# Kernel tuning notes

Measured on AMD Instinct MI355X. Metric: run time of the kernel, lower is better.

## Reference

```python
import jax, jax.numpy as jnp
import numpy as np

SIZE = 161          # odd box size (init arg 160 -> 161)
INPUT_SIZE = 8
BATCH = 256
MARGIN = 3          # VOXEL_SPREAD_MARGIN


def _radial_expansion(grid):
    # verbatim numpy port of SparseVolumeReconstructionLinear.radial_expansion
    bz = grid.shape[0]
    bz2 = bz // 2
    mask1 = grid == -1
    ls = np.linspace(-bz2, bz2, bz)
    lsx = np.linspace(0, bz2, bz // 2 + 1)
    z, y, x = np.meshgrid(ls, ls, lsx)
    c = np.zeros((int(np.sum(mask1)), 3))
    c[:, 0] = x[mask1]
    c[:, 1] = y[mask1]
    c[:, 2] = z[mask1]
    norm = np.sqrt(np.sum(np.square(c), axis=1))
    c_ = np.round(c / norm[:, None]).astype(int)
    c = c.astype(int)
    c[:, 1:] += bz2
    c_ = c - c_
    g = grid[c_[:, 2], c_[:, 1], c_[:, 0]]
    mask2 = g >= 0
    grid[c[mask2, 2], c[mask2, 1], c[mask2, 0]] = g[mask2]


def _build_grid3d_index(size):
    bz = size
    bz_2 = bz // 2
    zz = (np.arange(bz) - bz_2) ** 2
    yy = (np.arange(bz) - bz_2) ** 2
    xx = np.arange(bz_2 + 1) ** 2
    mask = (zz[:, None, None] + yy[None, :, None] + xx[None, None, :]) <= bz_2 ** 2
    # C-order enumeration matches grid_iterator(z, y, x) ordering
    idx = np.cumsum(mask.ravel()).reshape(mask.shape) - 1
    grid = np.where(mask, idx, -1).astype(np.int64)
    m = MARGIN
    bzm = bz + 2 * m
    gm = np.full((bzm, bzm, bzm // 2 + 1), -1, dtype=np.int64)
    gm[m:-m, m:-m, :-m] = grid
    for _ in range(5):
        _radial_expansion(gm)
    return gm, int(mask.sum())


def _rand_rotations(key, n):
    q = jax.random.normal(key, (n, 4))
    q = q / jnp.linalg.norm(q, axis=1, keepdims=True)
    w, x, y, z = q[:, 0], q[:, 1], q[:, 2], q[:, 3]
    R = jnp.stack([
        1 - 2 * (y * y + z * z), 2 * (x * y - z * w), 2 * (x * z + y * w),
        2 * (x * y + z * w), 1 - 2 * (x * x + z * z), 2 * (y * z - x * w),
        2 * (x * z - y * w), 2 * (y * z + x * w), 1 - 2 * (x * x + y * y),
    ], axis=-1).reshape(n, 3, 3)
    return R.astype(jnp.float32)


def setup_inputs() -> dict:
    key = jax.random.key(0)
    k1, k2, k3, k4 = jax.random.split(key, 4)
    grid3d_index, weight_count = _build_grid3d_index(SIZE)
    weight = jax.random.normal(k1, (weight_count, INPUT_SIZE, 2), dtype=jnp.float32) * 1e-3
    bias = jax.random.normal(k2, (weight_count, 2), dtype=jnp.float32) * 1e-3
    inp = jax.random.normal(k3, (BATCH, INPUT_SIZE), dtype=jnp.float32)
    rot = _rand_rotations(k4, BATCH)
    # half-plane 2D Fourier coords (x >= 0), P = SIZE * (SIZE//2 + 1)
    ys, xs = np.meshgrid(np.arange(SIZE) - SIZE // 2, np.arange(SIZE // 2 + 1), indexing='ij')
    coord = np.stack([xs.ravel(), ys.ravel()], axis=-1).astype(np.float32)
    return {
        'input': inp,
        'weight': weight,
        'bias': bias,
        'grid3d_index': jnp.asarray(grid3d_index),
        'rot_matrices': rot,
        'grid2d_coord': jnp.asarray(coord),
        'max_r': SIZE // 2,
    }


def reference(input, weight, bias, grid3d_index, rot_matrices, grid2d_coord, max_r):
    # input: (B, D); weight: (W, D, 2); bias: (W, 2)
    # grid2d_coord: (P, 2) as (x, y); rot_matrices: (B, 3, 3)
    bz = grid3d_index.shape[0]
    bz2 = bz // 2
    mr = min(int(max_r), (bz - 2 * MARGIN) // 2)
    P = grid2d_coord.shape[0]
    # rotate the z=0 plane into 3D Fourier space: (B, P, 3) as (x, y, z)
    c2 = jnp.pad(grid2d_coord, ((0, 0), (0, 1)))
    c = jnp.einsum('bij,pj->bpi', rot_matrices, c2)
    # Hermitian symmetry: flip to x >= 0 half-grid, conjugate
    flip = c[..., 0] < 0
    c = jnp.where(flip[..., None], -c, c)
    valid = jnp.sum(grid2d_coord ** 2, axis=-1) <= float(mr * mr)  # (P,)
    c = jnp.where(valid[None, :, None], c, 0.0)
    f = jnp.floor(c)
    t = c - f                      # trilinear fractions (B, P, 3)
    fi = f.astype(jnp.int32)
    out = jnp.zeros((c.shape[0], P, 2), dtype=input.dtype)
    for dx in (0, 1):
        wx = t[..., 0] if dx else 1.0 - t[..., 0]
        for dy in (0, 1):
            wy = t[..., 1] if dy else 1.0 - t[..., 1]
            for dz in (0, 1):
                wz = t[..., 2] if dz else 1.0 - t[..., 2]
                xi = fi[..., 0] + dx
                yi = fi[..., 1] + dy + bz2
                zi = fi[..., 2] + dz + bz2
                j = grid3d_index[zi, yi, xi]        # (B, P) voxel ids, -1 = empty
                jm = jnp.maximum(j, 0)
                v = jnp.einsum('bd,bpdc->bpc', input, weight[jm]) + bias[jm]
                v = jnp.where((j >= 0)[..., None], v, 0.0)
                out = out + (wx * wy * wz)[..., None] * v
    imag_sign = jnp.where(flip, -1.0, 1.0)
    out = out * jnp.stack([jnp.ones_like(imag_sign), imag_sign], axis=-1)
    return jnp.where(valid[None, :, None], out, 0.0)
```

## Files before the change

kernel.cpp:

```cpp
#include <hip/hip_runtime.h>

#define BZ    167
#define BZ2   83
#define NX    84
#define NCELL (BZ * BZ * NX)
#define NBX   51
#define NBX2  102

static __device__ __forceinline__ unsigned f2bf(float f) {
    unsigned u = __float_as_uint(f);
    return (u + 0x7FFFu + ((u >> 16) & 1u)) >> 16;
}
static __device__ __forceinline__ float bf_lo(unsigned u) {
    return __uint_as_float(u << 16);
}
static __device__ __forceinline__ float bf_hi(unsigned u) {
    return __uint_as_float(u & 0xFFFF0000u);
}

__global__ __launch_bounds__(256) void pack_all(
    const float4* __restrict__ wsrc, uint2* __restrict__ wdst, int nw4, int nbw,
    const int* __restrict__ grid, const float* __restrict__ bias,
    int2* __restrict__ garr, int ncell)
{
    if ((int)blockIdx.x < nbw) {
        const int i = blockIdx.x * 256 + threadIdx.x;
        if (i >= nw4) return;
        const float4 v = wsrc[i];
        wdst[i] = make_uint2(f2bf(v.x) | (f2bf(v.y) << 16),
                             f2bf(v.z) | (f2bf(v.w) << 16));
    } else {
        const int i = ((int)blockIdx.x - nbw) * 256 + threadIdx.x;
        if (i >= ncell) return;
        const int j = grid[i];
        unsigned bb = 0u;
        if (j >= 0)
            bb = f2bf(bias[2 * j]) | (f2bf(bias[2 * j + 1]) << 16);
        garr[i] = make_int2(j, (int)bb);
    }
}

__global__ __launch_bounds__(256, 4) void svr_half(
    const float*    __restrict__ input,
    const unsigned* __restrict__ wpk,
    const int2*     __restrict__ garr,
    const float*    __restrict__ rot,
    const float*    __restrict__ coord,
    const int*      __restrict__ max_r,
    float*          __restrict__ out,
    int P)
{
    const int m    = blockIdx.x;
    const int xcd  = m & 7;
    const int slot = m >> 3;
    const int b    = (slot / NBX2) * 8 + xcd;
    const int lane = threadIdx.x;
    const int half = lane & 1;
    const int p    = (slot % NBX2) * 128 + (lane >> 1);
    if (p >= P) return;

    const float2 xy = *(const float2*)(coord + 2 * p);
    const float x = xy.x, y = xy.y;

    const int mr = min(max_r[0], (BZ - 6) / 2);
    const bool valid = (x * x + y * y) <= (float)(mr * mr);

    float* o = out + (((size_t)b * P + p) * 2 + half);
    if (!valid) {
        *o = 0.f;
        return;
    }

    const float* R = rot + b * 9;
    float cx = fmaf(R[1], y, R[0] * x);
    float cy = fmaf(R[4], y, R[3] * x);
    float cz = fmaf(R[7], y, R[6] * x);

    float sgn = 1.f;
    if (cx < 0.f) { cx = -cx; cy = -cy; cz = -cz; sgn = -1.f; }

    const float fx = floorf(cx), fy = floorf(cy), fz = floorf(cz);
    const float tx = cx - fx, ty = cy - fy, tz = cz - fz;
    const int ix = (int)fx;
    const int iy = (int)fy + BZ2;
    const int iz = (int)fz + BZ2;

    const float4 ih = *(const float4*)(input + b * 8 + half * 4);

    int2 G[8];
    #pragma unroll
    for (int dz = 0; dz < 2; ++dz) {
        #pragma unroll
        for (int dy = 0; dy < 2; ++dy) {
            const int base = ((iz + dz) * BZ + (iy + dy)) * NX + ix;
            const int c = dz * 4 + dy * 2;
            G[c + 0] = garr[base + 0];
            G[c + 1] = garr[base + 1];
        }
    }

    int   jj[8];
    float wc[8];
    {
        const float wx0 = 1.f - tx, wy0 = 1.f - ty, wz0 = 1.f - tz;
        #pragma unroll
        for (int c = 0; c < 8; ++c) {
            const int dx = c & 1, dy = (c >> 1) & 1, dz = c >> 2;
            const float w = (dx ? tx : wx0) * (dy ? ty : wy0) * (dz ? tz : wz0);
            const int j = G[c].x;
            wc[c] = (j >= 0) ? w : 0.f;
            jj[c] = max(j, 0);
        }
    }

    uint4 U[8];
    #pragma unroll
    for (int c = 0; c < 8; ++c)
        U[c] = *(const uint4*)(wpk + (size_t)jj[c] * 8 + half * 4);

    float acc0 = 0.f, acc1 = 0.f;
    #pragma unroll
    for (int c = 0; c < 8; ++c) {
        const float w = wc[c];
        const unsigned bb = (unsigned)G[c].y;
        float v0 = half ? 0.f : bf_lo(bb);
        float v1 = half ? 0.f : bf_hi(bb);
        v0 = fmaf(ih.x, bf_lo(U[c].x), v0); v1 = fmaf(ih.x, bf_hi(U[c].x), v1);
        v0 = fmaf(ih.y, bf_lo(U[c].y), v0); v1 = fmaf(ih.y, bf_hi(U[c].y), v1);
        v0 = fmaf(ih.z, bf_lo(U[c].z), v0); v1 = fmaf(ih.z, bf_hi(U[c].z), v1);
        v0 = fmaf(ih.w, bf_lo(U[c].w), v0); v1 = fmaf(ih.w, bf_hi(U[c].w), v1);
        acc0 = fmaf(w, v0, acc0);
        acc1 = fmaf(w, v1, acc1);
    }

    const float t0 = acc0 + __shfl_xor(acc0, 1);
    const float t1 = (acc1 + __shfl_xor(acc1, 1)) * sgn;
    *o = half ? t1 : t0;
}

__global__ __launch_bounds__(256) void pack_w(
    const float4* __restrict__ src, uint2* __restrict__ dst, int n)
{
    const int i = blockIdx.x * 256 + threadIdx.x;
    if (i >= n) return;
    const float4 v = src[i];
    dst[i] = make_uint2(f2bf(v.x) | (f2bf(v.y) << 16),
                        f2bf(v.z) | (f2bf(v.w) << 16));
}
__global__ __launch_bounds__(256) void pack_b(
    const float* __restrict__ bias, unsigned* __restrict__ bpk, int W)
{
    const int j = blockIdx.x * 256 + threadIdx.x;
    if (j >= W) return;
    bpk[j] = f2bf(bias[2 * j]) | (f2bf(bias[2 * j + 1]) << 16);
}

__global__ __launch_bounds__(256) void svr_bf16(
    const float* __restrict__ input, const unsigned* __restrict__ wpk,
    const unsigned* __restrict__ bpk, const int* __restrict__ grid3d,
    const float* __restrict__ rot, const float* __restrict__ coord,
    const int* __restrict__ max_r, float* __restrict__ out, int P)
{
    const int m    = blockIdx.x;
    const int xcd  = m & 7;
    const int slot = m >> 3;
    const int b    = (slot / NBX) * 8 + xcd;
    const int p    = (slot % NBX) * 256 + threadIdx.x;
    if (p >= P) return;

    const float x = coord[2 * p + 0];
    const float y = coord[2 * p + 1];
    const int mr = min(max_r[0], (BZ - 6) / 2);
    const bool valid = (x * x + y * y) <= (float)(mr * mr);
    float2* o = (float2*)(out + ((size_t)b * P + p) * 2);
    if (!valid) { *o = make_float2(0.f, 0.f); return; }

    const float* R = rot + b * 9;
    float cx = fmaf(R[1], y, R[0] * x);
    float cy = fmaf(R[4], y, R[3] * x);
    float cz = fmaf(R[7], y, R[6] * x);
    float sgn = 1.f;
    if (cx < 0.f) { cx = -cx; cy = -cy; cz = -cz; sgn = -1.f; }
    const float fx = floorf(cx), fy = floorf(cy), fz = floorf(cz);
    const float tx = cx - fx, ty = cy - fy, tz = cz - fz;
    const int ix = (int)fx, iy = (int)fy + BZ2, iz = (int)fz + BZ2;

    const float* ib = input + b * 8;
    const float in0 = ib[0], in1 = ib[1], in2 = ib[2], in3 = ib[3];
    const float in4 = ib[4], in5 = ib[5], in6 = ib[6], in7 = ib[7];

    int jj[8]; float wc[8];
    const float wx0 = 1.f - tx, wy0 = 1.f - ty, wz0 = 1.f - tz;
    #pragma unroll
    for (int dz = 0; dz < 2; ++dz)
        #pragma unroll
        for (int dy = 0; dy < 2; ++dy) {
            const int base = ((iz + dz) * BZ + (iy + dy)) * NX + ix;
            #pragma unroll
            for (int dx = 0; dx < 2; ++dx) {
                const int c = dz * 4 + dy * 2 + dx;
                const int j = grid3d[base + dx];
                const float w = (dx ? tx : wx0) * (dy ? ty : wy0) * (dz ? tz : wz0);
                wc[c] = (j >= 0) ? w : 0.f;
                jj[c] = max(j, 0);
            }
        }

    uint4 U0[8], U1[8]; unsigned BB[8];
    #pragma unroll
    for (int c = 0; c < 8; ++c) {
        const uint4* wp = (const uint4*)(wpk + (size_t)jj[c] * 8);
        U0[c] = wp[0]; U1[c] = wp[1]; BB[c] = bpk[jj[c]];
    }

    float acc0 = 0.f, acc1 = 0.f;
    #pragma unroll
    for (int c = 0; c < 8; ++c) {
        const float w = wc[c];
        float v0 = bf_lo(BB[c]), v1 = bf_hi(BB[c]);
        v0 = fmaf(in0, bf_lo(U0[c].x), v0); v1 = fmaf(in0, bf_hi(U0[c].x), v1);
        v0 = fmaf(in1, bf_lo(U0[c].y), v0); v1 = fmaf(in1, bf_hi(U0[c].y), v1);
        v0 = fmaf(in2, bf_lo(U0[c].z), v0); v1 = fmaf(in2, bf_hi(U0[c].z), v1);
        v0 = fmaf(in3, bf_lo(U0[c].w), v0); v1 = fmaf(in3, bf_hi(U0[c].w), v1);
        v0 = fmaf(in4, bf_lo(U1[c].x), v0); v1 = fmaf(in4, bf_hi(U1[c].x), v1);
        v0 = fmaf(in5, bf_lo(U1[c].y), v0); v1 = fmaf(in5, bf_hi(U1[c].y), v1);
        v0 = fmaf(in6, bf_lo(U1[c].z), v0); v1 = fmaf(in6, bf_hi(U1[c].z), v1);
        v0 = fmaf(in7, bf_lo(U1[c].w), v0); v1 = fmaf(in7, bf_hi(U1[c].w), v1);
        acc0 = fmaf(w, v0, acc0);
        acc1 = fmaf(w, v1, acc1);
    }
    *o = make_float2(acc0, acc1 * sgn);
}

__global__ __launch_bounds__(256) void svr_fp32(
    const float* __restrict__ input, const float* __restrict__ weight,
    const float* __restrict__ bias, const int* __restrict__ grid3d,
    const float* __restrict__ rot, const float* __restrict__ coord,
    const int* __restrict__ max_r, float* __restrict__ out, int P)
{
    const int m    = blockIdx.x;
    const int xcd  = m & 7;
    const int slot = m >> 3;
    const int b    = (slot / NBX) * 8 + xcd;
    const int p    = (slot % NBX) * 256 + threadIdx.x;
    if (p >= P) return;

    const float x = coord[2 * p + 0];
    const float y = coord[2 * p + 1];
    const int mr = min(max_r[0], (BZ - 6) / 2);
    const bool valid = (x * x + y * y) <= (float)(mr * mr);
    float2* o = (float2*)(out + ((size_t)b * P + p) * 2);
    if (!valid) { *o = make_float2(0.f, 0.f); return; }

    const float* R = rot + b * 9;
    float cx = fmaf(R[1], y, R[0] * x);
    float cy = fmaf(R[4], y, R[3] * x);
    float cz = fmaf(R[7], y, R[6] * x);
    float sgn = 1.f;
    if (cx < 0.f) { cx = -cx; cy = -cy; cz = -cz; sgn = -1.f; }
    const float fx = floorf(cx), fy = floorf(cy), fz = floorf(cz);
    const float tx = cx - fx, ty = cy - fy, tz = cz - fz;
    const int ix = (int)fx, iy = (int)fy + BZ2, iz = (int)fz + BZ2;

    const float* ib = input + b * 8;
    const float in0 = ib[0], in1 = ib[1], in2 = ib[2], in3 = ib[3];
    const float in4 = ib[4], in5 = ib[5], in6 = ib[6], in7 = ib[7];

    int jj[8]; float wc[8];
    const float wx0 = 1.f - tx, wy0 = 1.f - ty, wz0 = 1.f - tz;
    #pragma unroll
    for (int dz = 0; dz < 2; ++dz)
        #pragma unroll
        for (int dy = 0; dy < 2; ++dy) {
            const int base = ((iz + dz) * BZ + (iy + dy)) * NX + ix;
            #pragma unroll
            for (int dx = 0; dx < 2; ++dx) {
                const int c = dz * 4 + dy * 2 + dx;
                const int j = grid3d[base + dx];
                const float w = (dx ? tx : wx0) * (dy ? ty : wy0) * (dz ? tz : wz0);
                wc[c] = (j >= 0) ? w : 0.f;
                jj[c] = max(j, 0);
            }
        }

    float acc0 = 0.f, acc1 = 0.f;
    #pragma unroll
    for (int c = 0; c < 8; ++c) {
        const size_t j = (size_t)jj[c];
        const float4* wp = (const float4*)(weight + j * 16);
        const float4 W0 = wp[0], W1 = wp[1], W2 = wp[2], W3 = wp[3];
        const float2 bb = *(const float2*)(bias + j * 2);
        const float w = wc[c];
        float v0 = bb.x, v1 = bb.y;
        v0 = fmaf(in0, W0.x, v0); v1 = fmaf(in0, W0.y, v1);
        v0 = fmaf(in1, W0.z, v0); v1 = fmaf(in1, W0.w, v1);
        v0 = fmaf(in2, W1.x, v0); v1 = fmaf(in2, W1.y, v1);
        v0 = fmaf(in3, W1.z, v0); v1 = fmaf(in3, W1.w, v1);
        v0 = fmaf(in4, W2.x, v0); v1 = fmaf(in4, W2.y, v1);
        v0 = fmaf(in5, W2.z, v0); v1 = fmaf(in5, W2.w, v1);
        v0 = fmaf(in6, W3.x, v0); v1 = fmaf(in6, W3.y, v1);
        v0 = fmaf(in7, W3.z, v0); v1 = fmaf(in7, W3.w, v1);
        acc0 = fmaf(w, v0, acc0);
        acc1 = fmaf(w, v1, acc1);
    }
    *o = make_float2(acc0, acc1 * sgn);
}

extern "C" void kernel_launch(void* const* d_in, const int* in_sizes, int n_in,
                              void* d_out, int out_size, void* d_ws, size_t ws_size,
                              hipStream_t stream) {
    const float* input  = (const float*)d_in[0];
    const float* weight = (const float*)d_in[1];
    const float* bias   = (const float*)d_in[2];
    const int*   grid3d = (const int*)  d_in[3];
    const float* rot    = (const float*)d_in[4];
    const float* coord  = (const float*)d_in[5];
    const int*   max_r  = (const int*)  d_in[6];
    float* out = (float*)d_out;

    const int P = in_sizes[5] / 2;
    const int B = in_sizes[4] / 9;
    const int W = in_sizes[1] / 16;

    const size_t wpk_bytes  = (size_t)W * 32;
    const size_t garr_bytes = (size_t)NCELL * 8;
    const size_t need_full  = wpk_bytes + garr_bytes;
    const size_t need_bf    = (size_t)W * 36;

    dim3 block(256, 1, 1);

    if (ws_size >= need_full) {
        unsigned* wpk = (unsigned*)d_ws;
        int2* garr = (int2*)((char*)d_ws + wpk_bytes);
        const int nw4 = W * 4;
        const int nbw = (nw4 + 255) / 256;
        const int nbg = (NCELL + 255) / 256;
        pack_all<<<nbw + nbg, block, 0, stream>>>(
            (const float4*)weight, (uint2*)wpk, nw4, nbw,
            grid3d, bias, garr, NCELL);
        dim3 grid(NBX2 * B, 1, 1);
        svr_half<<<grid, block, 0, stream>>>(input, wpk, garr, rot, coord,
                                             max_r, out, P);
    } else if (ws_size >= need_bf) {
        unsigned* wpk = (unsigned*)d_ws;
        unsigned* bpk = wpk + (size_t)W * 8;
        const int nw = W * 4;
        pack_w<<<(nw + 255) / 256, block, 0, stream>>>(
            (const float4*)weight, (uint2*)wpk, nw);
        pack_b<<<(W + 255) / 256, block, 0, stream>>>(bias, bpk, W);
        dim3 grid(NBX * B, 1, 1);
        svr_bf16<<<grid, block, 0, stream>>>(input, wpk, bpk, grid3d, rot,
                                             coord, max_r, out, P);
    } else {
        dim3 grid(NBX * B, 1, 1);
        svr_fp32<<<grid, block, 0, stream>>>(input, weight, bias, grid3d, rot,
                                             coord, max_r, out, P);
    }
}
```

Baseline: 234.7 us.

## Split each output point across four lanes with paired x-neighbor grid table

Adds a new path in which each output point is handled by four lanes: two for the x-neighbor and two for each half of the input dimension. A shuffle reduction combines the partial sums. A new packing kernel builds a 16-byte table that stores the voxel id and packed bias for a cell and its +x neighbor, so the four y/z corners need only four gathers. This is meant to raise parallelism and cut serial gather latency per thread. In exchange the grid table doubles in size and the pack pass does more work.

```diff
diff --git a/kernel.cpp b/kernel.cpp
--- a/kernel.cpp
+++ b/kernel.cpp
@@ -6,6 +6,7 @@
 #define NCELL (BZ * BZ * NX)
 #define NBX   51
 #define NBX2  102
+#define NBQ   204
 
 static __device__ __forceinline__ unsigned f2bf(float f) {
     unsigned u = __float_as_uint(f);
@@ -16,6 +17,131 @@
 }
 static __device__ __forceinline__ float bf_hi(unsigned u) {
     return __uint_as_float(u & 0xFFFF0000u);
+}
+
+__global__ __launch_bounds__(256) void pack_all2(
+    const float4* __restrict__ wsrc, uint2* __restrict__ wdst, int nw4, int nbw,
+    const int* __restrict__ grid, const float* __restrict__ bias,
+    int4* __restrict__ gpair, int ncell)
+{
+    if ((int)blockIdx.x < nbw) {
+        const int i = blockIdx.x * 256 + threadIdx.x;
+        if (i >= nw4) return;
+        const float4 v = wsrc[i];
+        wdst[i] = make_uint2(f2bf(v.x) | (f2bf(v.y) << 16),
+                             f2bf(v.z) | (f2bf(v.w) << 16));
+    } else {
+        const int i = ((int)blockIdx.x - nbw) * 256 + threadIdx.x;
+        if (i >= ncell) return;
+        const int j0 = grid[i];
+        const int j1 = (i + 1 < ncell) ? grid[i + 1] : -1;
+        unsigned b0 = 0u, b1 = 0u;
+        if (j0 >= 0)
+            b0 = f2bf(bias[2 * j0]) | (f2bf(bias[2 * j0 + 1]) << 16);
+        if (j1 >= 0)
+            b1 = f2bf(bias[2 * j1]) | (f2bf(bias[2 * j1 + 1]) << 16);
+        gpair[i] = make_int4(j0, (int)b0, j1, (int)b1);
+    }
+}
+
+__global__ __launch_bounds__(256, 4) void svr_quad(
+    const float*    __restrict__ input,
+    const unsigned* __restrict__ wpk,
+    const int4*     __restrict__ gpair,
+    const float*    __restrict__ rot,
+    const float*    __restrict__ coord,
+    const int*      __restrict__ max_r,
+    float*          __restrict__ out,
+    int P)
+{
+    const int m    = blockIdx.x;
+    const int xcd  = m & 7;
+    const int slot = m >> 3;
+    const int b    = (slot / NBQ) * 8 + xcd;
+    const int lane = threadIdx.x;
+    const int q    = lane & 3;
+    const int h    = q & 1;
+    const int dxl  = q >> 1;
+    const int p    = (slot % NBQ) * 64 + (lane >> 2);
+    if (p >= P) return;
+
+    const float2 xy = *(const float2*)(coord + 2 * p);
+    const float x = xy.x, y = xy.y;
+
+    const int mr = min(max_r[0], (BZ - 6) / 2);
+    const bool valid = (x * x + y * y) <= (float)(mr * mr);
+
+    float2* o = (float2*)(out + ((size_t)b * P + p) * 2);
+    if (!valid) {
+        if (q == 0) *o = make_float2(0.f, 0.f);
+        return;
+    }
+
+    const float* R = rot + b * 9;
+    float cx = fmaf(R[1], y, R[0] * x);
+    float cy = fmaf(R[4], y, R[3] * x);
+    float cz = fmaf(R[7], y, R[6] * x);
+
+    float sgn = 1.f;
+    if (cx < 0.f) { cx = -cx; cy = -cy; cz = -cz; sgn = -1.f; }
+
+    const float fx = floorf(cx), fy = floorf(cy), fz = floorf(cz);
+    const float tx = cx - fx, ty = cy - fy, tz = cz - fz;
+    const int ix = (int)fx;
+    const int iy = (int)fy + BZ2;
+    const int iz = (int)fz + BZ2;
+
+    int4 Gp[4];
+    #pragma unroll
+    for (int i = 0; i < 4; ++i) {
+        const int dy = i & 1, dz = i >> 1;
+        Gp[i] = gpair[((iz + dz) * BZ + (iy + dy)) * NX + ix];
+    }
+
+    const float4 ih = *(const float4*)(input + b * 8 + h * 4);
+
+    const float wxd = dxl ? tx : 1.f - tx;
+    float wyz[4];
+    wyz[0] = (1.f - ty) * (1.f - tz);
+    wyz[1] = ty * (1.f - tz);
+    wyz[2] = (1.f - ty) * tz;
+    wyz[3] = ty * tz;
+
+    int jj[4]; unsigned bbl[4]; float wcl[4];
+    #pragma unroll
+    for (int i = 0; i < 4; ++i) {
+        const int j = dxl ? Gp[i].z : Gp[i].x;
+        bbl[i] = (unsigned)(dxl ? Gp[i].w : Gp[i].y);
+        wcl[i] = (j >= 0) ? wxd * wyz[i] : 0.f;
+        jj[i]  = max(j, 0);
+    }
+
+    uint4 U[4];
+    #pragma unroll
+    for (int i = 0; i < 4; ++i)
+        U[i] = *(const uint4*)(wpk + (size_t)jj[i] * 8 + h * 4);
+
+    float acc0 = 0.f, acc1 = 0.f;
+    #pragma unroll
+    for (int i = 0; i < 4; ++i) {
+        const float w = wcl[i];
+        const unsigned bb = bbl[i];
+        float v0 = h ? 0.f : bf_lo(bb);
+        float v1 = h ? 0.f : bf_hi(bb);
+        v0 = fmaf(ih.x, bf_lo(U[i].x), v0); v1 = fmaf(ih.x, bf_hi(U[i].x), v1);
+        v0 = fmaf(ih.y, bf_lo(U[i].y), v0); v1 = fmaf(ih.y, bf_hi(U[i].y), v1);
+        v0 = fmaf(ih.z, bf_lo(U[i].z), v0); v1 = fmaf(ih.z, bf_hi(U[i].z), v1);
+        v0 = fmaf(ih.w, bf_lo(U[i].w), v0); v1 = fmaf(ih.w, bf_hi(U[i].w), v1);
+        acc0 = fmaf(w, v0, acc0);
+        acc1 = fmaf(w, v1, acc1);
+    }
+
+    acc0 += __shfl_xor(acc0, 1);
+    acc1 += __shfl_xor(acc1, 1);
+    acc0 += __shfl_xor(acc0, 2);
+    acc1 += __shfl_xor(acc1, 2);
+
+    if (q == 0) *o = make_float2(acc0, acc1 * sgn);
 }
 
 __global__ __launch_bounds__(256) void pack_all(
@@ -323,13 +449,25 @@
     const int W = in_sizes[1] / 16;
 
     const size_t wpk_bytes  = (size_t)W * 32;
-    const size_t garr_bytes = (size_t)NCELL * 8;
-    const size_t need_full  = wpk_bytes + garr_bytes;
+    const size_t need_quad  = wpk_bytes + (size_t)NCELL * 16;
+    const size_t need_full  = wpk_bytes + (size_t)NCELL * 8;
     const size_t need_bf    = (size_t)W * 36;
 
     dim3 block(256, 1, 1);
 
-    if (ws_size >= need_full) {
+    if (ws_size >= need_quad) {
+        unsigned* wpk = (unsigned*)d_ws;
+        int4* gpair = (int4*)((char*)d_ws + wpk_bytes);
+        const int nw4 = W * 4;
+        const int nbw = (nw4 + 255) / 256;
+        const int nbg = (NCELL + 255) / 256;
+        pack_all2<<<nbw + nbg, block, 0, stream>>>(
+            (const float4*)weight, (uint2*)wpk, nw4, nbw,
+            grid3d, bias, gpair, NCELL);
+        dim3 grid(NBQ * B, 1, 1);
+        svr_quad<<<grid, block, 0, stream>>>(input, wpk, gpair, rot, coord,
+                                             max_r, out, P);
+    } else if (ws_size >= need_full) {
         unsigned* wpk = (unsigned*)d_ws;
         int2* garr = (int2*)((char*)d_ws + wpk_bytes);
         const int nw4 = W * 4;
```

Measured after the change: 234.1 us. Within noise of the previous version (-0.3%).

## Split each output point across four lanes by x-corner and input half

Applied to the files above, without the earlier changes.

Each point is now handled by four lanes instead of two. Each lane gathers the four grid cells for one x-offset of the trilinear cube and one half of the input channels, and a two-step shuffle reduction combines the partial sums. A single lane writes the point's two outputs as one float2. This doubles thread and block count to expose more parallelism for the latency-bound gathers and to cut per-thread registers, at the cost of redundant rotation and coordinate math, and lanes loading adjacent x cells instead of one lane loading both.

```diff
diff --git a/kernel.cpp b/kernel.cpp
--- a/kernel.cpp
+++ b/kernel.cpp
@@ -5,7 +5,7 @@
 #define NX    84
 #define NCELL (BZ * BZ * NX)
 #define NBX   51
-#define NBX2  102
+#define NBQ   204
 
 static __device__ __forceinline__ unsigned f2bf(float f) {
     unsigned u = __float_as_uint(f);
@@ -40,7 +40,7 @@
     }
 }
 
-__global__ __launch_bounds__(256, 4) void svr_half(
+__global__ __launch_bounds__(256, 4) void svr_quad(
     const float*    __restrict__ input,
     const unsigned* __restrict__ wpk,
     const int2*     __restrict__ garr,
@@ -53,10 +53,12 @@
     const int m    = blockIdx.x;
     const int xcd  = m & 7;
     const int slot = m >> 3;
-    const int b    = (slot / NBX2) * 8 + xcd;
+    const int b    = (slot / NBQ) * 8 + xcd;
     const int lane = threadIdx.x;
-    const int half = lane & 1;
-    const int p    = (slot % NBX2) * 128 + (lane >> 1);
+    const int q    = lane & 3;
+    const int h    = q & 1;
+    const int dxl  = q >> 1;
+    const int p    = (slot % NBQ) * 64 + (lane >> 2);
     if (p >= P) return;
 
     const float2 xy = *(const float2*)(coord + 2 * p);
@@ -65,9 +67,9 @@
     const int mr = min(max_r[0], (BZ - 6) / 2);
     const bool valid = (x * x + y * y) <= (float)(mr * mr);
 
-    float* o = out + (((size_t)b * P + p) * 2 + half);
+    float2* o = (float2*)(out + ((size_t)b * P + p) * 2);
     if (!valid) {
-        *o = 0.f;
+        if (q == 0) *o = make_float2(0.f, 0.f);
         return;
     }
 
@@ -85,57 +87,56 @@
     const int iy = (int)fy + BZ2;
     const int iz = (int)fz + BZ2;
 
-    const float4 ih = *(const float4*)(input + b * 8 + half * 4);
-
-    int2 G[8];
-    #pragma unroll
-    for (int dz = 0; dz < 2; ++dz) {
-        #pragma unroll
-        for (int dy = 0; dy < 2; ++dy) {
-            const int base = ((iz + dz) * BZ + (iy + dy)) * NX + ix;
-            const int c = dz * 4 + dy * 2;
-            G[c + 0] = garr[base + 0];
-            G[c + 1] = garr[base + 1];
-        }
-    }
-
-    int   jj[8];
-    float wc[8];
-    {
-        const float wx0 = 1.f - tx, wy0 = 1.f - ty, wz0 = 1.f - tz;
-        #pragma unroll
-        for (int c = 0; c < 8; ++c) {
-            const int dx = c & 1, dy = (c >> 1) & 1, dz = c >> 2;
-            const float w = (dx ? tx : wx0) * (dy ? ty : wy0) * (dz ? tz : wz0);
-            const int j = G[c].x;
-            wc[c] = (j >= 0) ? w : 0.f;
-            jj[c] = max(j, 0);
-        }
-    }
-
-    uint4 U[8];
-    #pragma unroll
-    for (int c = 0; c < 8; ++c)
-        U[c] = *(const uint4*)(wpk + (size_t)jj[c] * 8 + half * 4);
+    const int base0 = (iz * BZ + iy) * NX + ix + dxl;
+    int2 Gl[4];
+    Gl[0] = garr[base0];
+    Gl[1] = garr[base0 + NX];
+    Gl[2] = garr[base0 + NX * BZ];
+    Gl[3] = garr[base0 + NX * BZ + NX];
+
+    const float4 ih = *(const float4*)(input + b * 8 + h * 4);
+
+    const float wxd = dxl ? tx : 1.f - tx;
+    float wyz[4];
+    wyz[0] = (1.f - ty) * (1.f - tz);
+    wyz[1] = ty * (1.f - tz);
+    wyz[2] = (1.f - ty) * tz;
+    wyz[3] = ty * tz;
+
+    int jj[4]; float wcl[4];
+    #pragma unroll
+    for (int i = 0; i < 4; ++i) {
+        const int j = Gl[i].x;
+        wcl[i] = (j >= 0) ? wxd * wyz[i] : 0.f;
+        jj[i]  = max(j, 0);
+    }
+
+    uint4 U[4];
+    #pragma unroll
+    for (int i = 0; i < 4; ++i)
+        U[i] = *(const uint4*)(wpk + (size_t)jj[i] * 8 + h * 4);
 
     float acc0 = 0.f, acc1 = 0.f;
     #pragma unroll
-    for (int c = 0; c < 8; ++c) {
-        const float w = wc[c];
-        const unsigned bb = (unsigned)G[c].y;
-        float v0 = half ? 0.f : bf_lo(bb);
-        float v1 = half ? 0.f : bf_hi(bb);
-        v0 = fmaf(ih.x, bf_lo(U[c].x), v0); v1 = fmaf(ih.x, bf_hi(U[c].x), v1);
-        v0 = fmaf(ih.y, bf_lo(U[c].y), v0); v1 = fmaf(ih.y, bf_hi(U[c].y), v1);
-        v0 = fmaf(ih.z, bf_lo(U[c].z), v0); v1 = fmaf(ih.z, bf_hi(U[c].z), v1);
-        v0 = fmaf(ih.w, bf_lo(U[c].w), v0); v1 = fmaf(ih.w, bf_hi(U[c].w), v1);
+    for (int i = 0; i < 4; ++i) {
+        const float w = wcl[i];
+        const unsigned bb = (unsigned)Gl[i].y;
+        float v0 = h ? 0.f : bf_lo(bb);
+        float v1 = h ? 0.f : bf_hi(bb);
+        v0 = fmaf(ih.x, bf_lo(U[i].x), v0); v1 = fmaf(ih.x, bf_hi(U[i].x), v1);
+        v0 = fmaf(ih.y, bf_lo(U[i].y), v0); v1 = fmaf(ih.y, bf_hi(U[i].y), v1);
+        v0 = fmaf(ih.z, bf_lo(U[i].z), v0); v1 = fmaf(ih.z, bf_hi(U[i].z), v1);
+        v0 = fmaf(ih.w, bf_lo(U[i].w), v0); v1 = fmaf(ih.w, bf_hi(U[i].w), v1);
         acc0 = fmaf(w, v0, acc0);
         acc1 = fmaf(w, v1, acc1);
     }
 
-    const float t0 = acc0 + __shfl_xor(acc0, 1);
-    const float t1 = (acc1 + __shfl_xor(acc1, 1)) * sgn;
-    *o = half ? t1 : t0;
+    acc0 += __shfl_xor(acc0, 1);
+    acc1 += __shfl_xor(acc1, 1);
+    acc0 += __shfl_xor(acc0, 2);
+    acc1 += __shfl_xor(acc1, 2);
+
+    if (q == 0) *o = make_float2(acc0, acc1 * sgn);
 }
 
 __global__ __launch_bounds__(256) void pack_w(
@@ -338,8 +339,8 @@
         pack_all<<<nbw + nbg, block, 0, stream>>>(
             (const float4*)weight, (uint2*)wpk, nw4, nbw,
             grid3d, bias, garr, NCELL);
-        dim3 grid(NBX2 * B, 1, 1);
-        svr_half<<<grid, block, 0, stream>>>(input, wpk, garr, rot, coord,
+        dim3 grid(NBQ * B, 1, 1);
+        svr_quad<<<grid, block, 0, stream>>>(input, wpk, garr, rot, coord,
                                              max_r, out, P);
     } else if (ws_size >= need_bf) {
         unsigned* wpk = (unsigned*)d_ws;
```

Result: no change. 232.6 us (-0.9%).
